# Performance work log

Hardware: AMD Instinct MI355X
Metric: run time of the kernel (lower is better)

Reference implementation:

```python
import jax, jax.numpy as jnp
import numpy as np

M, N, B, L = 512, 2048, 4, 20
H_DENSITY = 0.02  # Tanner graph sparsity: row weight ~N*p=40, col weight ~M*p=10


def setup_inputs() -> dict:
    key = jax.random.key(0)
    ks = jax.random.split(key, 10)
    H = jax.random.bernoulli(ks[0], H_DENSITY, (M, N)).astype(jnp.float32)
    llrs = jax.random.uniform(ks[1], (N,), jnp.float32)
    syndromes = jax.random.randint(ks[2], (B, M, 1), 0, 2, jnp.int32)
    errors = jax.random.randint(ks[3], (B, N), 0, 2, jnp.int32)
    weights_de = jax.random.uniform(ks[4], (L, M, N), jnp.float32)
    weights_llr = jax.random.uniform(ks[5], (L, N), jnp.float32)
    marg_weights_de = jax.random.uniform(ks[6], (L, M, N), jnp.float32)
    marg_weights_llr = jax.random.uniform(ks[7], (L, N), jnp.float32)
    rhos = jnp.ones((L,), jnp.float32)
    residual_weights = jnp.zeros((L,), jnp.float32)
    return dict(syndromes=syndromes, errors=errors, H=H, llrs=llrs,
                weights_de=weights_de, weights_llr=weights_llr,
                marg_weights_de=marg_weights_de, marg_weights_llr=marg_weights_llr,
                rhos=rhos, residual_weights=residual_weights)


def reference(syndromes, errors, H, llrs, weights_de, weights_llr,
              marg_weights_de, marg_weights_llr, rhos, residual_weights):
    batch = syndromes.shape[0]
    m, n = H.shape
    rhos_norm = jax.nn.softmax(rhos)                       # (L,)
    sign = 1.0 - 2.0 * syndromes.astype(H.dtype)           # (B,m,1): (-1)**syndrome
    err_f = errors.astype(H.dtype)                         # (B,n)
    eps = 1e-6

    def step(msgs_dn, xs):
        w_de, w_llr, mw_de, mw_llr, rho, rw = xs
        # error-node (variable) update: column-sum minus self, masked by H
        msgs_en = (H * (llrs * w_llr)
                   + jnp.sum(msgs_dn * w_de, axis=1, keepdims=True)) * H - msgs_dn
        # detector-node (check) update: tanh-product rule with self-exclusion
        d = jnp.tanh(msgs_en * 0.5)
        d = jnp.where(d == 0, jnp.asarray(1.0, d.dtype), d)
        d = jnp.clip(d, -1.0 + eps, 1.0 - eps)
        row_prod = jnp.prod(d, axis=2, keepdims=True)      # (B,m,1)
        msgs_new = 2.0 * jnp.arctanh(row_prod / d) * (sign * H) + rw * msgs_dn
        # marginal beliefs and weighted BCE loss
        beliefs = jnp.sum(msgs_new * mw_de, axis=1) + llrs * mw_llr   # (B,n)
        loss_b = jnp.sum(jax.nn.softplus(beliefs) - (1.0 - err_f) * beliefs, axis=1)
        return msgs_new, rho * loss_b

    init = jnp.zeros((batch, m, n), H.dtype)
    _, losses = jax.lax.scan(
        step, init,
        (weights_de, weights_llr, marg_weights_de, marg_weights_llr,
         rhos_norm, residual_weights))
    return jnp.sum(losses) / batch
```

## Files before the change

### kernel.cpp

```cpp
#include <hip/hip_runtime.h>

#define MM 512
#define NN 2048
#define BB 4
#define LL 20
#define MAXDEG 128
#define NT    1024
#define NBLK  32
#define RR    8
#define COLSB 256
#define SLOTS 4096
#define EPSV  1e-6f

#define WS_ROW_DEG   0
#define WS_ROW_PAD   2048
#define WS_ROW_OFFF  264192
#define WS_RPTR_RB   266240
#define WS_EDGE_CS   282880
#define WS_WDE_P     413952
#define WS_MWDE_P    3035392
#define WS_PP        5656832
#define WS_BAR       5787904

__device__ __forceinline__ void pre_barrier(int* ctr) {
    __syncthreads();
    if (threadIdx.x == 0) {
        __threadfence();
        __hip_atomic_fetch_add(ctr, 1, __ATOMIC_RELAXED, __HIP_MEMORY_SCOPE_AGENT);
        int it = 0;
        while (__hip_atomic_load(ctr, __ATOMIC_RELAXED, __HIP_MEMORY_SCOPE_AGENT) < NBLK) {
            __builtin_amdgcn_s_sleep(1);
            if (++it > (1 << 22)) break;
        }
        __threadfence();
    }
    __syncthreads();
}

__device__ __forceinline__ void grid_barrier(int* ctr) {
    __syncthreads();
    if (threadIdx.x == 0) {
        asm volatile("s_waitcnt vmcnt(0)" ::: "memory");
        __hip_atomic_fetch_add(ctr, 1, __ATOMIC_RELAXED, __HIP_MEMORY_SCOPE_AGENT);
        int it = 0;
        while (__hip_atomic_load(ctr, __ATOMIC_RELAXED, __HIP_MEMORY_SCOPE_AGENT) < RR) {
            __builtin_amdgcn_s_sleep(1);
            if (++it > (1 << 22)) break;
        }
        asm volatile("" ::: "memory");
    }
    __syncthreads();
}

__global__ __launch_bounds__(NT, 4)
void nbp_all(const int* __restrict__ synd, const int* __restrict__ errs,
             const float* __restrict__ H, const float* __restrict__ llrs,
             const float* __restrict__ w_de, const float* __restrict__ w_llr,
             const float* __restrict__ mw_de, const float* __restrict__ mw_llr,
             const float* __restrict__ rhos, const float* __restrict__ resw,
             int* __restrict__ row_deg, int* __restrict__ row_pad,
             float* __restrict__ row_offf, int* __restrict__ rptr_rb,
             unsigned* __restrict__ edge_cs,
             float* __restrict__ wde_p, float* __restrict__ mwde_p,
             float* __restrict__ pp, int* __restrict__ bar,
             float* __restrict__ out) {
    __shared__ float d_sb[SLOTS];
    __shared__ int   tmp_s[MM];
    __shared__ float colsum_s[COLSB];
    __shared__ float bel_s[COLSB];
    __shared__ float ncs_s[COLSB];
    __shared__ float llrs_s[COLSB];
    __shared__ float ef_s[COLSB];
    __shared__ float rowprod_s[MM];
    __shared__ float rp_coef[MM];
    __shared__ int   rowptr_s[MM + 1];
    __shared__ float rho_n[LL];
    __shared__ float red[16];

    const int blk = blockIdx.x;
    const int b = blk & 3, r = blk >> 2;
    const int tid = threadIdx.x;
    const int lane = tid & 63, wave = tid >> 6;
    int* bar_b = bar + b * 64;
    int* pbar  = bar + BB * 64;

    {
        int i = blk * 16 + wave;
        const float* hrow = H + (size_t)i * NN;
        int base = 0;
        for (int pass = 0; pass < 4; ++pass) {
            float v[8];
            #pragma unroll
            for (int c = 0; c < 8; ++c) v[c] = hrow[(pass * 8 + c) * 64 + lane];
            #pragma unroll
            for (int c = 0; c < 8; ++c) {
                bool pred = v[c] != 0.0f;
                unsigned long long mask = __ballot(pred);
                int before = __popcll(mask & ((1ull << lane) - 1ull));
                if (pred) {
                    int k = base + before;
                    if (k < MAXDEG) row_pad[i * MAXDEG + k] = (pass * 8 + c) * 64 + lane;
                }
                base += __popcll(mask);
            }
        }
        if (lane == 0) {
            row_deg[i] = base < MAXDEG ? base : MAXDEG;
            row_offf[i] = powf(1.0f - EPSV, (float)(NN - base));
        }
    }
    pre_barrier(&pbar[0]);

    if (blk < RR) {
        const int slice = blk;
        if (tid < MM) {
            int deg = row_deg[tid], cnt = 0;
            for (int k = 0; k < deg; ++k)
                cnt += ((row_pad[tid * MAXDEG + k] >> 8) == slice);
            tmp_s[tid] = cnt;
        }
        __syncthreads();
        for (int off = 1; off < MM; off <<= 1) {
            int v = (tid < MM && tid >= off) ? tmp_s[tid - off] : 0;
            __syncthreads();
            if (tid < MM) tmp_s[tid] += v;
            __syncthreads();
        }
        if (tid == 0) rptr_rb[slice * 513] = 0;
        if (tid < MM) rptr_rb[slice * 513 + tid + 1] = tmp_s[tid];
        __syncthreads();
        if (tid < MM) {
            int deg = row_deg[tid];
            int pos = (tid == 0) ? 0 : tmp_s[tid - 1];
            for (int k = 0; k < deg; ++k) {
                int c = row_pad[tid * MAXDEG + k];
                if ((c >> 8) == slice && pos < SLOTS) {
                    edge_cs[slice * SLOTS + pos] = ((unsigned)tid << 16) | (unsigned)c;
                    ++pos;
                }
            }
        }
    }
    pre_barrier(&pbar[1]);

    {
        int tot = rptr_rb[r * 513 + MM];
        if (tot > SLOTS) tot = SLOTS;
        for (int l = b * 5; l < b * 5 + 5; ++l) {
            for (int s = tid; s < SLOTS; s += NT) {
                size_t di = ((size_t)(l * RR + r)) * SLOTS + s;
                if (s < tot) {
                    unsigned pk = edge_cs[r * SLOTS + s];
                    size_t src = (size_t)l * MM * NN + (size_t)(pk >> 16) * NN + (pk & 0xffffu);
                    wde_p[di]  = w_de[src];
                    mwde_p[di] = mw_de[src];
                } else {
                    wde_p[di]  = 0.0f;
                    mwde_p[di] = 0.0f;
                }
            }
        }
    }
    pre_barrier(&pbar[2]);

    if (tid == 0) {
        float mx = -1e30f;
        for (int l = 0; l < LL; ++l) mx = fmaxf(mx, rhos[l]);
        float s = 0.0f;
        for (int l = 0; l < LL; ++l) { float e = __expf(rhos[l] - mx); rho_n[l] = e; s += e; }
        for (int l = 0; l < LL; ++l) rho_n[l] /= s;
    }
    if (tid < MM) {
        rowptr_s[tid] = rptr_rb[r * 513 + tid];
        rp_coef[tid] = row_offf[tid] * (1.0f - 2.0f * (float)synd[b * MM + tid]);
    }
    if (tid == MM) rowptr_s[MM] = rptr_rb[r * 513 + MM];
    if (tid < COLSB) {
        int j = r * COLSB + tid;
        float lj = llrs[j];
        llrs_s[tid] = lj;
        colsum_s[tid] = lj * w_llr[j];
        ef_s[tid] = 1.0f - (float)errs[b * NN + j];
        bel_s[tid] = 0.0f;
        ncs_s[tid] = 0.0f;
    }

    int cnt = rptr_rb[r * 513 + MM];
    if (cnt > SLOTS) cnt = SLOTS;
    const int s0 = 4 * tid;

    unsigned idx[4];
    float msg[4], d_r[4];
    #pragma unroll
    for (int k = 0; k < 4; ++k) {
        int e = r * SLOTS + s0 + k;
        idx[k] = edge_cs[(s0 + k) < cnt ? e : r * SLOTS];
        msg[k] = 0.0f;
    }
    __syncthreads();

    float loss = 0.0f;

    for (int l = 0; l < LL; ++l) {
        const float rw = resw[l];
        const int par = l & 1;
        float* pp_b = pp + ((size_t)par * BB + b) * RR * MM;

        const float4 mq = *(const float4*)(mwde_p + ((size_t)(l * RR + r) * SLOTS) + s0);
        float4 wq = make_float4(0.f, 0.f, 0.f, 0.f);
        if (l + 1 < LL)
            wq = *(const float4*)(wde_p + ((size_t)((l + 1) * RR + r) * SLOTS) + s0);
        const float mv[4] = {mq.x, mq.y, mq.z, mq.w};
        const float wn[4] = {wq.x, wq.y, wq.z, wq.w};

        #pragma unroll
        for (int k = 0; k < 4; ++k) {
            int jl = idx[k] & 255u;
            float en = colsum_s[jl] - msg[k];
            float t = __expf(en);
            float d = 1.0f - 2.0f * __builtin_amdgcn_rcpf(t + 1.0f);
            if (d == 0.0f) d = 1.0f;
            d = fminf(fmaxf(d, -1.0f + EPSV), 1.0f - EPSV);
            d_r[k] = d;
        }
        *(float4*)&d_sb[s0] = make_float4(d_r[0], d_r[1], d_r[2], d_r[3]);
        __syncthreads();

        if (tid < MM) {
            int lo = rowptr_s[tid], hi = rowptr_s[tid + 1];
            if (hi > SLOTS) hi = SLOTS;
            float p = 1.0f;
            for (int s = lo; s < hi; ++s) p *= d_sb[s];
            __hip_atomic_store(&pp_b[r * MM + tid], p,
                               __ATOMIC_RELAXED, __HIP_MEMORY_SCOPE_AGENT);
        }
        grid_barrier(&bar_b[l]);

        if (tid < MM) {
            float p = rp_coef[tid];
            #pragma unroll
            for (int r2 = 0; r2 < RR; ++r2)
                p *= __hip_atomic_load(&pp_b[r2 * MM + tid],
                                       __ATOMIC_RELAXED, __HIP_MEMORY_SCOPE_AGENT);
            rowprod_s[tid] = p;
        }
        __syncthreads();

        #pragma unroll
        for (int k = 0; k < 4; ++k) {
            int il = idx[k] >> 16;
            int jl = idx[k] & 255u;
            float rq = rowprod_s[il] * __builtin_amdgcn_rcpf(d_r[k]);
            float v = __logf(1.0f + rq) - __logf(1.0f - rq) + rw * msg[k];
            msg[k] = v;
            if (s0 + k < cnt) {
                atomicAdd(&bel_s[jl], v * mv[k]);
                if (l + 1 < LL) atomicAdd(&ncs_s[jl], v * wn[k]);
            }
        }
        __syncthreads();

        if (tid < COLSB) {
            int j = r * COLSB + tid;
            float bel = llrs_s[tid] * mw_llr[l * NN + j] + bel_s[tid];
            bel_s[tid] = 0.0f;
            float sp = fmaxf(bel, 0.0f) + log1pf(__expf(-fabsf(bel)));
            loss += rho_n[l] * (sp - ef_s[tid] * bel);
            if (l + 1 < LL) {
                colsum_s[tid] = llrs_s[tid] * w_llr[(l + 1) * NN + j] + ncs_s[tid];
                ncs_s[tid] = 0.0f;
            }
        }
        __syncthreads();
    }

    #pragma unroll
    for (int off = 32; off > 0; off >>= 1) loss += __shfl_down(loss, off);
    if (lane == 0) red[wave] = loss;
    __syncthreads();
    if (wave == 0) {
        float v = (lane < 16) ? red[lane] : 0.0f;
        #pragma unroll
        for (int off = 8; off > 0; off >>= 1) v += __shfl_down(v, off);
        if (lane == 0) atomicAdd(out, v * 0.25f);
    }
}

extern "C" void kernel_launch(void* const* d_in, const int* in_sizes, int n_in,
                              void* d_out, int out_size, void* d_ws, size_t ws_size,
                              hipStream_t stream) {
    const int*   synd  = (const int*)  d_in[0];
    const int*   errs  = (const int*)  d_in[1];
    const float* H     = (const float*)d_in[2];
    const float* llrs  = (const float*)d_in[3];
    const float* w_de  = (const float*)d_in[4];
    const float* w_llr = (const float*)d_in[5];
    const float* mw_de = (const float*)d_in[6];
    const float* mw_llr= (const float*)d_in[7];
    const float* rhos  = (const float*)d_in[8];
    const float* resw  = (const float*)d_in[9];

    char* ws = (char*)d_ws;
    int*      row_deg  = (int*)     (ws + WS_ROW_DEG);
    int*      row_pad  = (int*)     (ws + WS_ROW_PAD);
    float*    row_offf = (float*)   (ws + WS_ROW_OFFF);
    int*      rptr_rb  = (int*)     (ws + WS_RPTR_RB);
    unsigned* edge_cs  = (unsigned*)(ws + WS_EDGE_CS);
    float*    wde_p    = (float*)   (ws + WS_WDE_P);
    float*    mwde_p   = (float*)   (ws + WS_MWDE_P);
    float*    pp       = (float*)   (ws + WS_PP);
    int*      bar      = (int*)     (ws + WS_BAR);
    float*    out      = (float*)d_out;

    hipMemsetAsync(bar, 0, (BB * 64 + 64) * sizeof(int), stream);
    hipMemsetAsync(d_out, 0, sizeof(float), stream);

    nbp_all<<<NBLK, NT, 0, stream>>>(synd, errs, H, llrs, w_de, w_llr, mw_de, mw_llr,
                                     rhos, resw, row_deg, row_pad, row_offf, rptr_rb,
                                     edge_cs, wde_p, mwde_p, pp, bar, out);
}
```

Before: 470.4 us.

## Double column slices to 64 blocks and gather weights directly each layer

Splits columns into 16 slices of 128, so 64 blocks run with 2 edges per thread instead of 32 blocks with 4. Drops the pre-pass that packed per-edge weights into workspace, along with one grid-wide barrier; each layer now gathers mw_de and next-layer w_de straight from the dense arrays by edge index. The output is zeroed inside the kernel instead of with a separate memset. The scattered uncoalesced gathers now sit on the critical path of every layer, and more blocks per batch join the per-layer grid barrier.

Result: faster. 439.5 us (-6.6%).

```diff
diff --git a/kernel.cpp b/kernel.cpp
--- a/kernel.cpp
+++ b/kernel.cpp
@@ -6,21 +6,20 @@
 #define LL 20
 #define MAXDEG 128
 #define NT    1024
-#define NBLK  32
-#define RR    8
-#define COLSB 256
-#define SLOTS 4096
+#define RR    16
+#define NBLK  64
+#define COLSB 128
+#define SLOTS 2048
+#define EPT   2
 #define EPSV  1e-6f
 
 #define WS_ROW_DEG   0
 #define WS_ROW_PAD   2048
 #define WS_ROW_OFFF  264192
 #define WS_RPTR_RB   266240
-#define WS_EDGE_CS   282880
-#define WS_WDE_P     413952
-#define WS_MWDE_P    3035392
-#define WS_PP        5656832
-#define WS_BAR       5787904
+#define WS_EDGE_CS   299072
+#define WS_PP        430144
+#define WS_BAR       692288
 
 __device__ __forceinline__ void pre_barrier(int* ctr) {
     __syncthreads();
@@ -52,7 +51,7 @@
     __syncthreads();
 }
 
-__global__ __launch_bounds__(NT, 4)
+__global__ __launch_bounds__(NT)
 void nbp_all(const int* __restrict__ synd, const int* __restrict__ errs,
              const float* __restrict__ H, const float* __restrict__ llrs,
              const float* __restrict__ w_de, const float* __restrict__ w_llr,
@@ -61,7 +60,6 @@
              int* __restrict__ row_deg, int* __restrict__ row_pad,
              float* __restrict__ row_offf, int* __restrict__ rptr_rb,
              unsigned* __restrict__ edge_cs,
-             float* __restrict__ wde_p, float* __restrict__ mwde_p,
              float* __restrict__ pp, int* __restrict__ bar,
              float* __restrict__ out) {
     __shared__ float d_sb[SLOTS];
@@ -84,8 +82,11 @@
     int* bar_b = bar + b * 64;
     int* pbar  = bar + BB * 64;
 
-    {
-        int i = blk * 16 + wave;
+    if (blk == 0 && tid == 0)
+        __hip_atomic_store(out, 0.0f, __ATOMIC_RELAXED, __HIP_MEMORY_SCOPE_AGENT);
+
+    if (wave < 8) {
+        int i = blk * 8 + wave;
         const float* hrow = H + (size_t)i * NN;
         int base = 0;
         for (int pass = 0; pass < 4; ++pass) {
@@ -116,7 +117,7 @@
         if (tid < MM) {
             int deg = row_deg[tid], cnt = 0;
             for (int k = 0; k < deg; ++k)
-                cnt += ((row_pad[tid * MAXDEG + k] >> 8) == slice);
+                cnt += ((row_pad[tid * MAXDEG + k] >> 7) == slice);
             tmp_s[tid] = cnt;
         }
         __syncthreads();
@@ -134,7 +135,7 @@
             int pos = (tid == 0) ? 0 : tmp_s[tid - 1];
             for (int k = 0; k < deg; ++k) {
                 int c = row_pad[tid * MAXDEG + k];
-                if ((c >> 8) == slice && pos < SLOTS) {
+                if ((c >> 7) == slice && pos < SLOTS) {
                     edge_cs[slice * SLOTS + pos] = ((unsigned)tid << 16) | (unsigned)c;
                     ++pos;
                 }
@@ -142,26 +143,6 @@
         }
     }
     pre_barrier(&pbar[1]);
-
-    {
-        int tot = rptr_rb[r * 513 + MM];
-        if (tot > SLOTS) tot = SLOTS;
-        for (int l = b * 5; l < b * 5 + 5; ++l) {
-            for (int s = tid; s < SLOTS; s += NT) {
-                size_t di = ((size_t)(l * RR + r)) * SLOTS + s;
-                if (s < tot) {
-                    unsigned pk = edge_cs[r * SLOTS + s];
-                    size_t src = (size_t)l * MM * NN + (size_t)(pk >> 16) * NN + (pk & 0xffffu);
-                    wde_p[di]  = w_de[src];
-                    mwde_p[di] = mw_de[src];
-                } else {
-                    wde_p[di]  = 0.0f;
-                    mwde_p[di] = 0.0f;
-                }
-            }
-        }
-    }
-    pre_barrier(&pbar[2]);
 
     if (tid == 0) {
         float mx = -1e30f;
@@ -187,12 +168,12 @@
 
     int cnt = rptr_rb[r * 513 + MM];
     if (cnt > SLOTS) cnt = SLOTS;
-    const int s0 = 4 * tid;
-
-    unsigned idx[4];
-    float msg[4], d_r[4];
+    const int s0 = EPT * tid;
+
+    unsigned idx[EPT];
+    float msg[EPT], d_r[EPT];
     #pragma unroll
-    for (int k = 0; k < 4; ++k) {
+    for (int k = 0; k < EPT; ++k) {
         int e = r * SLOTS + s0 + k;
         idx[k] = edge_cs[(s0 + k) < cnt ? e : r * SLOTS];
         msg[k] = 0.0f;
@@ -206,16 +187,21 @@
         const int par = l & 1;
         float* pp_b = pp + ((size_t)par * BB + b) * RR * MM;
 
-        const float4 mq = *(const float4*)(mwde_p + ((size_t)(l * RR + r) * SLOTS) + s0);
-        float4 wq = make_float4(0.f, 0.f, 0.f, 0.f);
-        if (l + 1 < LL)
-            wq = *(const float4*)(wde_p + ((size_t)((l + 1) * RR + r) * SLOTS) + s0);
-        const float mv[4] = {mq.x, mq.y, mq.z, mq.w};
-        const float wn[4] = {wq.x, wq.y, wq.z, wq.w};
+        float mv[EPT], wn[EPT];
+        {
+            const float* mwl = mw_de + (size_t)l * (MM * NN);
+            const float* wl  = w_de + (size_t)(l + 1) * (MM * NN);
+            #pragma unroll
+            for (int k = 0; k < EPT; ++k) {
+                size_t eo = (size_t)(idx[k] >> 16) * NN + (idx[k] & 0xffffu);
+                mv[k] = mwl[eo];
+                wn[k] = (l + 1 < LL) ? wl[eo] : 0.0f;
+            }
+        }
 
         #pragma unroll
-        for (int k = 0; k < 4; ++k) {
-            int jl = idx[k] & 255u;
+        for (int k = 0; k < EPT; ++k) {
+            int jl = idx[k] & (COLSB - 1);
             float en = colsum_s[jl] - msg[k];
             float t = __expf(en);
             float d = 1.0f - 2.0f * __builtin_amdgcn_rcpf(t + 1.0f);
@@ -223,7 +209,7 @@
             d = fminf(fmaxf(d, -1.0f + EPSV), 1.0f - EPSV);
             d_r[k] = d;
         }
-        *(float4*)&d_sb[s0] = make_float4(d_r[0], d_r[1], d_r[2], d_r[3]);
+        *(float2*)&d_sb[s0] = make_float2(d_r[0], d_r[1]);
         __syncthreads();
 
         if (tid < MM) {
@@ -247,9 +233,9 @@
         __syncthreads();
 
         #pragma unroll
-        for (int k = 0; k < 4; ++k) {
+        for (int k = 0; k < EPT; ++k) {
             int il = idx[k] >> 16;
-            int jl = idx[k] & 255u;
+            int jl = idx[k] & (COLSB - 1);
             float rq = rowprod_s[il] * __builtin_amdgcn_rcpf(d_r[k]);
             float v = __logf(1.0f + rq) - __logf(1.0f - rq) + rw * msg[k];
             msg[k] = v;
@@ -306,16 +292,13 @@
     float*    row_offf = (float*)   (ws + WS_ROW_OFFF);
     int*      rptr_rb  = (int*)     (ws + WS_RPTR_RB);
     unsigned* edge_cs  = (unsigned*)(ws + WS_EDGE_CS);
-    float*    wde_p    = (float*)   (ws + WS_WDE_P);
-    float*    mwde_p   = (float*)   (ws + WS_MWDE_P);
     float*    pp       = (float*)   (ws + WS_PP);
     int*      bar      = (int*)     (ws + WS_BAR);
     float*    out      = (float*)d_out;
 
     hipMemsetAsync(bar, 0, (BB * 64 + 64) * sizeof(int), stream);
-    hipMemsetAsync(d_out, 0, sizeof(float), stream);
 
     nbp_all<<<NBLK, NT, 0, stream>>>(synd, errs, H, llrs, w_de, w_llr, mw_de, mw_llr,
                                      rhos, resw, row_deg, row_pad, row_offf, rptr_rb,
-                                     edge_cs, wde_p, mwde_p, pp, bar, out);
+                                     edge_cs, pp, bar, out);
 }
```
